# Kernel tuning notes

Measured on AMD Instinct MI355X. Metric: run time of the kernel, lower is better.

Reference implementation:

```python
import jax, jax.numpy as jnp
import numpy as np

SC = 19          # window stride/size (non-kitti)
K = 3 * SC       # 57, unfold kernel size
CH = 128         # chnn

def conv2d(x, w, b=None, pad=(0, 0)):
    y = jax.lax.conv_general_dilated(
        x, w, (1, 1), [(pad[0], pad[0]), (pad[1], pad[1])],
        dimension_numbers=('NCHW', 'OIHW', 'NCHW'))
    return y if b is None else y + b[None, :, None, None]

def unfold(x):
    # nn.Unfold(kernel_size=3*SC, padding=SC, stride=SC) -> [b, c, K*K, h_sc*w_sc]
    b, c, h, w = x.shape
    h_sc, w_sc = h // SC, w // SC
    xp = jnp.pad(x, ((0, 0), (0, 0), (SC, SC), (SC, SC)))
    ii = np.arange(h_sc)[:, None] * SC + np.arange(K)[None, :]
    jj = np.arange(w_sc)[:, None] * SC + np.arange(K)[None, :]
    p = xp[:, :, ii, :][:, :, :, :, jj]              # [b,c,h_sc,K,w_sc,K]
    return p.transpose(0, 1, 3, 5, 2, 4).reshape(b, c, K * K, h_sc * w_sc)

def to_windows(x):
    # [b,c,h,w] -> [b,c,h_sc*w_sc, SC*SC] (non-overlapping SCxSC windows)
    b, c, h, w = x.shape
    h_sc, w_sc = h // SC, w // SC
    return x.reshape(b, c, h_sc, SC, w_sc, SC).transpose(0, 1, 2, 4, 3, 5).reshape(b, c, h_sc * w_sc, SC * SC)

def fs_kernel(w_prelu, b, h, w):
    # geometric falloff kernel, separable in x/y: [b, K*K, L, SC*SC]
    a = w_prelu[0] * 0.02      # scp = 0.02
    half = 2.0 * SC            # half_ker
    crd = jnp.arange(K, dtype=jnp.float32)
    idx_x = SC + jnp.arange(w, dtype=jnp.float32) % SC
    idx_y = SC + jnp.arange(h, dtype=jnp.float32) % SC
    def falloff(d):
        v = d - half
        pre = jnp.where(v > 0, v, a * v)   # PReLU
        return jnp.maximum(1.0 - pre, 0.0) # -prelu + b(=1), clamped at 0
    ox = falloff(jnp.abs(crd[:, None] - idx_x[None, :]))  # [K, w]
    oy = falloff(jnp.abs(crd[:, None] - idx_y[None, :]))  # [K, h]
    ker = oy[:, None, :, None] * ox[None, :, None, :]      # [Ky, Kx, h, w]
    ker = jnp.broadcast_to(ker[None], (b, K, K, h, w)).reshape(b, K * K, h, w)
    return to_windows(ker)

def kpa(feat_ci, feat_mi, w_qk, w_v, gamma, w_prelu):
    b, c, h_in, w_in = feat_mi.shape
    x_pad = SC - w_in % SC
    y_pad = SC - h_in % SC
    pad4 = ((0, 0), (0, 0), (0, y_pad), (0, x_pad))
    feat_c = jnp.pad(feat_ci, pad4)
    feat_m = jnp.pad(feat_mi, pad4)
    h, w = h_in + y_pad, w_in + x_pad
    h_sc, w_sc = h // SC, w // SC
    # validity mask -> additive -99 bias for padded keys/queries
    fm = jnp.pad(jnp.ones((1, 1, h_in, w_in), feat_mi.dtype), pad4)
    fm_k = unfold(fm)                                  # [1,1,K^2,L]
    fm_q = to_windows(fm)                              # [1,1,L,SC^2]
    am = (fm_k[:, 0, :, :, None] * fm_q[:, 0, None, :, :] - 1.0) * 99.0
    # itr == 0 path: compute attention
    qk = conv2d(feat_c, w_qk)
    feat_q, feat_k = qk[:, :c], qk[:, c:]
    feat_k = unfold(feat_k) * (c ** -0.5)              # [b,c,K^2,L]
    feat_q = to_windows(feat_q)                        # [b,c,L,SC^2]
    attn = jnp.einsum('bckn,bcns->bkns', feat_k, feat_q) + am
    attn = jax.nn.softmax(fs_kernel(w_prelu, b, h, w) * attn, axis=1)
    feat_v = unfold(conv2d(feat_m, w_v))               # [b,c,K^2,L]
    feat_r = jnp.einsum('bkns,bckn->bcns', attn, feat_v)  # [b,c,L,SC^2]
    feat_r = feat_r.reshape(b, c, h_sc, w_sc, SC, SC).transpose(0, 1, 2, 4, 3, 5).reshape(b, c, h, w)
    return feat_mi + feat_r[:, :, :h_in, :w_in] * gamma[0]

def sep_conv_gru(h, x, wz1, bz1, wr1, br1, wq1, bq1, wz2, bz2, wr2, br2, wq2, bq2):
    hx = jnp.concatenate([h, x], 1)
    z = jax.nn.sigmoid(conv2d(hx, wz1, bz1, (0, 2)))
    r = jax.nn.sigmoid(conv2d(hx, wr1, br1, (0, 2)))
    q = jnp.tanh(conv2d(jnp.concatenate([r * h, x], 1), wq1, bq1, (0, 2)))
    h = (1 - z) * h + z * q
    hx = jnp.concatenate([h, x], 1)
    z = jax.nn.sigmoid(conv2d(hx, wz2, bz2, (2, 0)))
    r = jax.nn.sigmoid(conv2d(hx, wr2, br2, (2, 0)))
    q = jnp.tanh(conv2d(jnp.concatenate([r * h, x], 1), wq2, bq2, (2, 0)))
    return (1 - z) * h + z * q

PARAM_SHAPES = [
    ('w_cor1', (256, 324, 1, 1)), ('b_cor1', (256,)), ('w_cor2', (192, 256, 3, 3)), ('b_cor2', (192,)),
    ('w_flo1', (128, 2, 7, 7)), ('b_flo1', (128,)), ('w_flo2', (64, 128, 3, 3)), ('b_flo2', (64,)),
    ('w_mo', (126, 256, 3, 3)), ('b_mo', (126,)),
    ('w_qk', (256, 128, 1, 1)), ('w_v', (128, 128, 1, 1)),
    ('wz1', (128, 512, 1, 5)), ('bz1', (128,)), ('wr1', (128, 512, 1, 5)), ('br1', (128,)),
    ('wq1', (128, 512, 1, 5)), ('bq1', (128,)),
    ('wz2', (128, 512, 5, 1)), ('bz2', (128,)), ('wr2', (128, 512, 5, 1)), ('br2', (128,)),
    ('wq2', (128, 512, 5, 1)), ('bq2', (128,)),
    ('w_f1', (256, 128, 3, 3)), ('b_f1', (256,)), ('w_f2', (2, 256, 3, 3)), ('b_f2', (2,)),
    ('w_m1', (256, 128, 3, 3)), ('b_m1', (256,)), ('w_m2', (576, 256, 1, 1)), ('b_m2', (576,)),
]

def setup_inputs() -> dict:
    key = jax.random.key(0)
    B, H, W = 2, 55, 128
    ks = jax.random.split(key, len(PARAM_SHAPES) + 4)
    inp = {
        'net': jax.random.normal(ks[0], (B, CH, H, W), jnp.float32),
        'inp': jax.random.normal(ks[1], (B, CH, H, W), jnp.float32),
        'corr': jax.random.normal(ks[2], (B, 324, H, W), jnp.float32),
        'flow': jax.random.normal(ks[3], (B, 2, H, W), jnp.float32),
    }
    for i, (name, shp) in enumerate(PARAM_SHAPES):
        fan_in = int(np.prod(shp[1:])) if len(shp) > 1 else shp[0]
        scale = 1.0 / np.sqrt(fan_in) if len(shp) > 1 else 0.01
        inp[name] = scale * jax.random.normal(ks[4 + i], shp, jnp.float32)
    inp['gamma'] = jnp.array([0.5], jnp.float32)            # nonzero so KPA contributes
    inp['w_prelu'] = jnp.array([1.0 / 28.0], jnp.float32)    # 1 / h_k, h_k = (3*SC-1)/2
    inp['itr'] = 0
    return inp

def reference(net, inp, corr, flow, w_cor1, b_cor1, w_cor2, b_cor2, w_flo1, b_flo1, w_flo2, b_flo2, w_mo, b_mo, w_qk, w_v, wz1, bz1, wr1, br1, wq1, bq1, wz2, bz2, wr2, br2, wq2, bq2, w_f1, b_f1, w_f2, b_f2, w_m1, b_m1, w_m2, b_m2, gamma, w_prelu, itr):
    # _mo_enc
    fc = jax.nn.relu(conv2d(corr, w_cor1, b_cor1))
    fc = jax.nn.relu(conv2d(fc, w_cor2, b_cor2, (1, 1)))
    ff = jax.nn.relu(conv2d(flow, w_flo1, b_flo1, (3, 3)))
    ff = jax.nn.relu(conv2d(ff, w_flo2, b_flo2, (1, 1)))
    fm = jax.nn.relu(conv2d(jnp.concatenate([fc, ff], 1), w_mo, b_mo, (1, 1)))
    feat_mo = jnp.concatenate([fm, flow], 1)           # [b,128,h,w]
    # KPA attention (itr == 0)
    feat_moa = kpa(inp, feat_mo, w_qk, w_v, gamma, w_prelu)
    x = jnp.concatenate([inp, feat_mo, feat_moa], 1)   # [b,384,h,w]
    net = sep_conv_gru(net, x, wz1, bz1, wr1, br1, wq1, bq1, wz2, bz2, wr2, br2, wq2, bq2)
    d = jax.nn.relu(conv2d(net, w_f1, b_f1, (1, 1)))
    delta_flow = conv2d(d, w_f2, b_f2, (1, 1))
    m = jax.nn.relu(conv2d(net, w_m1, b_m1, (1, 1)))
    mask = 0.25 * conv2d(m, w_m2, b_m2)
    return net, mask, delta_flow
```

## Files before the change

kernel.cpp:

```cpp
#include <hip/hip_runtime.h>
#include <hip/hip_bf16.h>

typedef __bf16 bf16;
typedef __attribute__((ext_vector_type(8))) __bf16 v8bf;
typedef __attribute__((ext_vector_type(4))) float f32x4;
typedef __attribute__((ext_vector_type(16))) float f32x16;

#define HH 55
#define WW 128
#define HWP 7040
#define BHW 14080
#define QS 0.08838834764831845f
#define LOG2E 1.4426950408889634f

__device__ __forceinline__ void g2l16(const bf16* g, bf16* l){
  __builtin_amdgcn_global_load_lds(
      (const __attribute__((address_space(1))) void*)g,
      (__attribute__((address_space(3))) void*)l, 16, 0, 0);
}

#define NCV 19
__device__ const int PK_srcCS[NCV]  = {324,256,128,256,128,128,512,512,512,512,512,512,128,128,256,256,98,512,512};
__device__ const int PK_csv[NCV]    = {324,256,128,256,128,128,512,512,128,512,512,128,128,128,256,256,98,384,384};
__device__ const int PK_srcOff[NCV] = {0,0,0,0,0,0,0,0,0,0,0,0,0,0,0,0,0,128,128};
__device__ const int PK_wsrc[NCV]   = {0,1,2,3,4,5,6,7,8,9,10,11,12,13,14,15,16,8,11};
__device__ const int PK_Kc[NCV]     = {384,256,128,256,128,128,512,512,128,512,512,128,128,128,256,256,128,384,384};
__device__ const int PK_ntap[NCV]   = {1,9,9,9,1,1,5,5,5,5,5,5,9,9,9,1,1,5,5};
__device__ const int PK_Ctot[NCV]   = {256,256,128,128,256,128,256,256,128,256,256,128,512,512,128,640,128,128,128};
__device__ const int PK_coB[NCV]    = {0,0,0,0,0,0,0,128,0,0,128,0,0,256,0,0,0,0,0};
__device__ const int PK_dst[NCV]    = {0,98304,688128,835584,1130496,1163264,1179648,1179648,
  1835008,2162688,2162688,2818048,3145728,3145728,3735552,4030464,4194304,1916928,2899968};
__device__ const int PKD_cum[NCV+1] = {0,98304,540672,614400,904704,937472,953856,
  1281536,1609216,1691136,2018816,2346496,2428416,2723328,3018240,3022848,3170304,
  3186688,3432448,3678208};
__device__ const int PKD_Co[NCV]    = {256,192,64,126,256,128,128,128,128,128,128,128,256,256,2,576,128,128,128};

__device__ const int PB_off[15]={0,256,512,640,1152,1280,1408,1536,1664,1792,1920,2176,2432,2560,3200};
__device__ const int PB_cnt[15]={256,192,64,126,128,128,128,128,128,128,256,256,2,576,128};

struct W17 { const float* w[17]; };
struct B15 { const float* b[15]; };

struct XP {
  W17 wp; B15 bp;
  const float *net, *inp, *corr, *flow;
  bf16 *Bp; float *bias;
  bf16 *hx; float *hcur; bf16 *corr_cl; bf16 *im2c;
};

__global__ __launch_bounds__(256) void init_k(XP X){
  __shared__ float T[64][65];
  int bid = blockIdx.x;
  const int t = threadIdx.x;
  if (bid < 14368){
    int idx = bid*256 + t;
    int c = 0;
    while (idx >= PKD_cum[c+1]) ++c;
    int local = idx - PKD_cum[c];
    if (c == 16){
      int co = local >> 7, k = local & 127;
      if (k < 98)
        X.Bp[PK_dst[16] + co*128 + k] = (bf16)X.wp.w[16][co*98 + (k&1)*49 + (k>>1)];
      return;
    }
    int Kc = PK_Kc[c];
    int CKc = PKD_Co[c]*Kc;
    int tap = local / CKc;
    int rem = local - tap*CKc;
    int co = rem / Kc;
    int ci = rem - co*Kc;
    if (ci < PK_csv[c]){
      float v = X.wp.w[PK_wsrc[c]][(co*PK_srcCS[c] + PK_srcOff[c] + ci)*PK_ntap[c] + tap];
      if (c == 4 && co < 128) v *= QS;
      X.Bp[PK_dst[c] + (tap*PK_Ctot[c] + PK_coB[c] + co)*Kc + ci] = (bf16)v;
    }
    return;
  }
  bid -= 14368;
  if (bid < 880){
    int pt = bid%110, ct = (bid/110)&3, b = bid/440;
    const float* src = (ct < 2) ? X.net : X.inp;
    int c0s = (ct & 1)*64;
    int cbase = (ct < 2) ? 0 : 128;
    int p0 = pt*64;
    int pj = t & 63, cr4 = t >> 6;
#pragma unroll
    for (int i=0;i<16;++i)
      T[cr4 + i*4][pj] = src[((size_t)b*128 + c0s + cr4 + i*4)*HWP + p0 + pj];
    __syncthreads();
    int cj = t & 63, pr4 = t >> 6;
#pragma unroll
    for (int i=0;i<16;++i){
      int pp = p0 + pr4 + i*4;
      float v = T[cj][pr4 + i*4];
      X.hx[((size_t)(b*HWP+pp))*512 + cbase + c0s + cj] = (bf16)v;
      if (ct < 2) X.hcur[((size_t)(b*HWP+pp))*128 + c0s + cj] = v;
    }
    return;
  }
  bid -= 880;
  if (bid < 1320){
    int pt = bid%110, ct = (bid/110)%6, b = bid/660;
    int p0 = pt*64, c0s = ct*64;
    int pj = t & 63, cr4 = t >> 6;
#pragma unroll
    for (int i=0;i<16;++i){
      int c = c0s + cr4 + i*4;
      float v = 0.f;
      if (c < 324) v = X.corr[((size_t)b*324 + c)*HWP + p0 + pj];
      T[cr4 + i*4][pj] = v;
    }
    __syncthreads();
    int cj = t & 63, pr4 = t >> 6;
#pragma unroll
    for (int i=0;i<16;++i){
      int pp = p0 + pr4 + i*4;
      int cc = c0s + cj;
      X.corr_cl[((size_t)(b*HWP+pp))*384 + cc] = (bf16)T[cj][pr4 + i*4];
    }
    return;
  }
  bid -= 1320;
  if (bid < 110){
    int i = bid*256 + t;
    int c = i & 1, p = i >> 1;
    int b = p / HWP, pix = p - b*HWP;
    X.hx[(size_t)p*512 + 382 + c] = (bf16)X.flow[(b*2+c)*HWP + pix];
    return;
  }
  bid -= 110;
  if (bid < 7040){
    int i = bid*256 + t;
    int k = i & 127, p = i >> 7;
    int b = p / HWP, pix = p - b*HWP, y = pix >> 7, x = pix & 127;
    float v = 0.f;
    if (k < 98){
      int tap = k >> 1, c2 = k & 1, kh = tap/7, kw = tap - 7*(tap/7);
      int yy = y + kh - 3, xx = x + kw - 3;
      if ((unsigned)yy < 55u && (unsigned)xx < 128u) v = X.flow[(b*2+c2)*HWP + yy*128 + xx];
    }
    X.im2c[i] = (bf16)v;
    return;
  }
  for (int e=0;e<15;++e)
    for (int o=t; o<PB_cnt[e]; o+=256)
      X.bias[PB_off[e]+o] = X.bp.b[e][o];
}

__global__ __launch_bounds__(256) void transp_v(
    const bf16* __restrict__ src, bf16* __restrict__ dst)
{
  int pt = blockIdx.x, ct = blockIdx.y, b = blockIdx.z;
  __shared__ unsigned short T[64][66];
  int t = threadIdx.x;
  int p0 = pt*64, c0s = ct*64;
  int cj = t & 63, pr4 = t >> 6;
#pragma unroll
  for (int i=0;i<16;++i){
    int pp = p0 + pr4 + i*4;
    T[cj][pr4 + i*4] = ((const unsigned short*)src)[((size_t)(b*HWP+pp))*128 + c0s + cj];
  }
  __syncthreads();
  int pj = t & 63, cr4 = t >> 6;
#pragma unroll
  for (int i=0;i<16;++i){
    int cc = c0s + cr4 + i*4;
    ((unsigned short*)dst)[((size_t)(b*128 + cc))*HWP + p0 + pj] = T[cr4 + i*4][pj];
  }
}

struct GP {
  const bf16* A; const bf16* A2;
  const bf16* Bp; const float* bias;
  void* outp; const float* auxZ; float* auxH; float* auxN; const float* auxQ;
  int Astride, A2stride, Asplit;
  int outCtot, outC0, Nvalid, Kc, CtotPad, tapcode, act, outmode, ntiles, ntOff;
  float scale;
};

__global__ __launch_bounds__(256) void gemm_conv(GP ga, GP gb, GP gc, const bf16* __restrict__ zp)
{
  const int Mt = blockIdx.x;
  int nt = blockIdx.y;
  GP g;
  if (nt < ga.ntiles){ g = ga; }
  else if (nt < ga.ntiles + gb.ntiles){ g = gb; nt -= ga.ntiles; }
  else { g = gc; nt -= ga.ntiles + gb.ntiles; }
  const bf16* A        = g.A;
  const bf16* A2       = g.A2;
  const bf16* Bp       = g.Bp;
  const float* bias    = g.bias;
  void* outp           = g.outp;
  const float* auxZ    = g.auxZ;
  float* auxH          = g.auxH;
  float* auxN          = g.auxN;
  const float* auxQ    = g.auxQ;
  const int Astride    = g.Astride;
  const int A2stride   = g.A2stride;
  const int Asplit     = g.Asplit;
  const int outCtot    = g.outCtot;
  const int outC0      = g.outC0;
  const int Nvalid     = g.Nvalid;
  const int Kc         = g.Kc;
  const int CtotPad    = g.CtotPad;
  const int tapcode    = g.tapcode;
  const int act        = g.act;
  const int outmode    = g.outmode;
  const int ntOff      = g.ntOff;
  const float scale    = g.scale;

  const int bimg = Mt/110;
  const int rem = Mt - bimg*110;
  const int yy0 = rem >> 1;
  const int xh  = (rem & 1) << 6;
  const int tid = threadIdx.x;
  const int lane = tid & 63, wave = tid >> 6;
  const int wm = wave >> 1, wn = wave & 1;
  const int lr = lane & 15, lq2 = lane >> 4;

  __shared__ __align__(16) bf16 Al[2][4096];
  __shared__ __align__(16) bf16 Bl[2][8192];

  f32x4 acc[2][4];
#pragma unroll
  for (int m=0;m<2;++m)
#pragma unroll
    for (int n=0;n<4;++n) acc[m][n] = (f32x4){0.f,0.f,0.f,0.f};

  const int ntap = (tapcode==0) ? 1 : (tapcode==1 ? 9 : 5);
  const int nsteps = ntap*(Kc>>6);

  const int srow = tid >> 3;
  const int sc   = tid & 7;

#define STAGE(BUF, T, KC) { \
    int ddy, ddx; \
    if (tapcode==0){ ddy=0; ddx=0; } \
    else if (tapcode==1){ ddy=(T)/3-1; ddx=(T)-3*((T)/3)-1; } \
    else if (tapcode==2){ ddy=0; ddx=(T)-2; } \
    else { ddy=(T)-2; ddx=0; } \
    int ysrc = yy0 + ddy; \
    bool yok = (unsigned)ysrc < 55u; \
    const bf16* Abase; int Astr; \
    if ((KC) < Asplit){ Astr = A2stride; \
      Abase = A2 + (size_t)((bimg*55+ysrc)*128)*Astr + (KC); } \
    else { Astr = Astride; \
      Abase = A + (size_t)((bimg*55+ysrc)*128)*Astr + (KC); } \
    _Pragma("unroll") \
    for (int is=0; is<2; ++is){ \
      int r = is*32 + srow; \
      int cc = sc ^ (r&7); \
      int gx = xh + r + ddx; \
      const bf16* srcp = (yok && (unsigned)gx < 128u) ? \
          (Abase + (size_t)gx*Astr + cc*8) : (zp + cc*8); \
      g2l16(srcp, &Al[BUF][is*2048 + wave*512]); \
    } \
    const bf16* Bt = Bp + (size_t)((T)*CtotPad + (nt+ntOff)*128)*Kc + (KC); \
    _Pragma("unroll") \
    for (int is=0; is<4; ++is){ \
      int r = is*32 + srow; \
      int cc = sc ^ (r&7); \
      g2l16(Bt + (size_t)r*Kc + cc*8, &Bl[BUF][is*2048 + wave*512]); \
    } }

  STAGE(0, 0, 0);
  __syncthreads();

  int tcur = 0, kcc = 0;
  for (int si=0; si<nsteps; ++si){
    int kn = kcc + 64, tn = tcur;
    if (kn == Kc){ kn = 0; tn = tcur + 1; }
    if (si + 1 < nsteps){ STAGE((si+1)&1, tn, kn); }
    __builtin_amdgcn_sched_barrier(0);
    kcc = kn; tcur = tn;
    const bf16* Ac = Al[si&1];
    const bf16* Bc = Bl[si&1];
#pragma unroll
    for (int kk=0; kk<2; ++kk){
      v8bf af[2], bfr[4];
#pragma unroll
      for (int m=0;m<2;++m){
        int row = wm*32 + m*16 + lr;
        af[m] = *(const v8bf*)(Ac + row*64 + (((kk*4+lq2) ^ (row&7))<<3));
      }
#pragma unroll
      for (int n=0;n<4;++n){
        int row = wn*64 + n*16 + lr;
        bfr[n] = *(const v8bf*)(Bc + row*64 + (((kk*4+lq2) ^ (row&7))<<3));
      }
#pragma unroll
      for (int m=0;m<2;++m)
#pragma unroll
        for (int n=0;n<4;++n)
          acc[m][n] = __builtin_amdgcn_mfma_f32_16x16x32_bf16(af[m], bfr[n], acc[m][n], 0,0,0);
    }
    __syncthreads();
  }
#undef STAGE

  const size_t pixbase = (size_t)(bimg*55 + yy0)*128 + xh;
  if (outmode == 0){
    bf16* Ost = (bf16*)Al;
#pragma unroll
    for (int nn=0; nn<4; ++nn){
      int colL = wn*64 + nn*16 + lr;
      float bvl = bias[(nt+ntOff)*128 + colL];
#pragma unroll
      for (int m=0;m<2;++m){
        int rowx = wm*32 + m*16 + lq2*4;
        f32x4 v = acc[m][nn];
#pragma unroll
        for (int r=0;r<4;++r){
          float vv = v[r] + bvl;
          if (act==1)      vv = fmaxf(vv, 0.f);
          else if (act==2) vv = 1.f/(1.f+__expf(-vv));
          else if (act==3) vv = tanhf(vv);
          vv *= scale;
          int row = rowx + r;
          int pch = (colL>>3) ^ (row & 7);
          Ost[row*128 + (pch<<3) + (colL&7)] = (bf16)vv;
        }
      }
    }
    __syncthreads();
    {
      int rowl = tid >> 2, seg = tid & 3;
      size_t p = pixbase + rowl;
      bf16* dstp = (bf16*)outp + p*outCtot + outC0 + (nt+ntOff)*128 + seg*32;
      const bf16* srcr = Ost + rowl*128;
      int cb = (nt+ntOff)*128 + seg*32;
#pragma unroll
      for (int k2=0;k2<4;++k2){
        int pch = (seg*4 + k2) ^ (rowl & 7);
        int cog = cb + k2*8;
        if (cog + 8 <= Nvalid)
          *(uint4*)(dstp + k2*8) = *(const uint4*)(srcr + (pch<<3));
        else if (cog < Nvalid){
          const bf16* s8 = srcr + (pch<<3);
          for (int e=0; e<Nvalid-cog; ++e) dstp[k2*8+e] = s8[e];
        }
      }
    }
  } else if (outmode == 2){
    float* Ost2 = (float*)Bl;
#pragma unroll
    for (int nn=0; nn<4; ++nn){
      int chL = wn*64 + nn*16 + lr;
      float bvl = bias[(nt+ntOff)*128 + chL];
#pragma unroll
      for (int m=0;m<2;++m){
        int rowx = wm*32 + m*16 + lq2*4;
        f32x4 v = acc[m][nn];
#pragma unroll
        for (int r=0;r<4;++r){
          float vv = v[r] + bvl;
          if (act==1)      vv = fmaxf(vv, 0.f);
          else if (act==2) vv = 1.f/(1.f+__expf(-vv));
          else if (act==3) vv = tanhf(vv);
          Ost2[chL*64 + rowx + r] = vv*scale;
        }
      }
    }
    __syncthreads();
    {
      int ch = tid >> 1, half = tid & 1;
      int cog = (nt+ntOff)*128 + ch;
      if (cog < Nvalid){
        float* dstp = (float*)outp + ((size_t)bimg*outCtot + outC0 + cog)*HWP
                    + yy0*128 + xh + half*32;
        const float* srcr = Ost2 + ch*64 + half*32;
#pragma unroll
        for (int k2=0;k2<8;++k2)
          *(uint4*)(dstp + k2*4) = *(const uint4*)(srcr + k2*4);
      }
    }
  } else {
#pragma unroll
    for (int nn=0; nn<4; ++nn){
      int cog = (nt+ntOff)*128 + wn*64 + nn*16 + lr;
      float bvl = bias[cog];
      bool cok = cog < Nvalid;
#pragma unroll
      for (int m=0;m<2;++m){
        int rowx = wm*32 + m*16 + lq2*4;
        f32x4 v = acc[m][nn];
#pragma unroll
        for (int r=0;r<4;++r){
          int prow = rowx + r;
          size_t p = pixbase + prow;
          float vv = v[r] + bvl;
          if (outmode==4 && auxQ) vv += auxQ[p*128 + cog];
          if (act==1)      vv = fmaxf(vv, 0.f);
          else if (act==2) vv = 1.f/(1.f+__expf(-vv));
          else if (act==3) vv = tanhf(vv);
          vv *= scale;
          if (cok){
            if (outmode==1) ((float*)outp)[p*outCtot + outC0 + cog] = vv;
            else if (outmode==3){
              int c = cog & 127;
              ((bf16*)outp)[p*128 + c] = (bf16)(vv * auxH[p*128 + c]);
            } else {
              int c = cog;
              float z  = auxZ[p*128 + c];
              float h0 = auxH[p*128 + c];
              float hn = (1.f - z)*h0 + z*vv;
              auxH[p*128 + c] = hn;
              ((bf16*)outp)[p*512 + c] = (bf16)hn;
              if (auxN){
                int pixloc = (int)(p - (size_t)bimg*HWP);
                auxN[((size_t)bimg*128 + c)*HWP + pixloc] = hn;
              }
            }
          }
        }
      }
    }
  }
}

__global__ __launch_bounds__(256,1) void attn_k(
    const bf16* __restrict__ QK, const bf16* __restrict__ Vt,
    bf16* __restrict__ hx,
    const float* __restrict__ gammap, const float* __restrict__ wprelup)
{
  __shared__ __align__(16) float SM[16640];
  const int tid = threadIdx.x;
  const int wv = tid >> 6, lane = tid & 63;
  const int lq = lane & 31, hi = lane >> 5;
  const int blk = blockIdx.x;
  const int qt = blk % 12;
  const int n  = (blk/12) % 21;
  const int b  = blk / 252;
  const int hs = n/7, wd = n - 7*hs;
  const int y0 = (hs-1)*19, x0 = (wd-1)*19;
  const int rylo = max(0, y0), ryhi = min(54, y0+56);
  const int rxlo = max(0, x0), rxhi = min(127, x0+56);
  const int rxA  = rxlo & ~7;
  const int s = qt*32 + lq;
  const int sy = s/19, sx = s - sy*19;
  const int qy = y0 + 19 + sy, qx = x0 + 19 + sx;
  const int qpix = (b*55 + min(qy,54))*128 + min(qx,127);
  const float a = wprelup[0]*0.02f;
  const float qyf = (float)qy;

  bf16* Kl = (bf16*)SM + wv*8192;
  bf16* Vl = Kl + 4096;

  v8bf qf[8];
#pragma unroll
  for (int ks=0; ks<8; ++ks)
    qf[ks] = *(const v8bf*)(QK + (size_t)qpix*256 + ks*16 + hi*8);

  float fx0[16], fx1[16];
  unsigned msk0 = 0, msk1 = 0;
  {
    float dxq0 = (float)(rxA - qx);
    int xl0 = rxlo - rxA, xm0 = rxhi - rxA;
#pragma unroll
    for (int r=0;r<16;++r){
      int Ri = (r&3) + 8*(r>>2) + 4*hi;
      float dxv = fabsf(dxq0 + (float)Ri) - 38.f;
      fx0[r] = fmaxf(1.f - fmaxf(dxv, a*dxv), 0.f);
      if (Ri >= xl0 && Ri <= xm0) msk0 |= 1u<<r;
      float dxv1 = fabsf(dxq0 + 32.f + (float)Ri) - 38.f;
      fx1[r] = fmaxf(1.f - fmaxf(dxv1, a*dxv1), 0.f);
      int Ri1 = Ri + 32;
      if (Ri1 >= xl0 && Ri1 <= xm0) msk1 |= 1u<<r;
    }
  }

  f32x16 acc[4];
#pragma unroll
  for (int nf=0; nf<4; ++nf)
#pragma unroll
    for (int r=0;r<16;++r) acc[nf][r] = 0.f;
  float m2 = -40.f, den = 0.f;

  const int nry = (ryhi - rylo - wv)/4 + 1;
  const int nit = nry*2;

#define ISSUE_K(RY, RX) { int pixK = (b*55+(RY))*128 + (RX); \
  _Pragma("unroll") \
  for (int i=0;i<8;++i){ \
    int key = i*4 + (lane>>4); int cs = (lane&15) ^ (key&7); \
    g2l16(QK + (size_t)(pixK+key)*256 + 128 + cs*8, Kl + i*512); } }
#define ISSUE_V(RY, RX) { \
  _Pragma("unroll") \
  for (int i=0;i<8;++i){ \
    int ch = i*16 + (lane>>2); int cs = (lane&3) ^ ((ch>>1)&3); \
    g2l16(Vt + (size_t)(b*128+ch)*HWP + (RY)*128 + (RX) + cs*8, Vl + i*512); } }

  ISSUE_K(rylo + wv, rxA);

  for (int it=0; it<nit; ++it){
    const int ry  = rylo + wv + (it>>1)*4;
    const int tpar = it & 1;
    asm volatile("s_waitcnt lgkmcnt(0)" ::: "memory");
    __builtin_amdgcn_sched_barrier(0);
    asm volatile("s_waitcnt vmcnt(0)" ::: "memory");
    __builtin_amdgcn_sched_barrier(0);
    ISSUE_V(ry, rxA + tpar*32);
    __builtin_amdgcn_sched_barrier(0);

    f32x16 Cs;
#pragma unroll
    for (int r=0;r<16;++r) Cs[r] = 0.f;
#pragma unroll
    for (int ks=0; ks<8; ++ks){
      v8bf kf = *(const v8bf*)(Kl + lq*128 + (((ks*2+hi) ^ (lq&7))<<3));
      Cs = __builtin_amdgcn_mfma_f32_32x32x16_bf16(kf, qf[ks], Cs, 0,0,0);
    }
    float pr[16];
    {
      float dyv = fabsf((float)ry - qyf) - 38.f;
      float fy = fmaxf(1.f - fmaxf(dyv, a*dyv), 0.f);
      float fyk = fy * LOG2E;
      unsigned mk = tpar ? msk1 : msk0;
      float l2v[16]; float tmax = -1e30f;
#pragma unroll
      for (int r=0;r<16;++r){
        float fx = tpar ? fx1[r] : fx0[r];
        float lv = fyk * fx * Cs[r];
        lv = ((mk>>r)&1u) ? lv : -1e30f;
        l2v[r] = lv;
        tmax = fmaxf(tmax, lv);
      }
      tmax = fmaxf(tmax, __shfl_xor(tmax, 32));
      if (__any(tmax > m2 + 11.f)){
        float m2n = fmaxf(m2, tmax);
        float sc = exp2f(m2 - m2n);
        den *= sc;
#pragma unroll
        for (int r=0;r<16;++r){
          float scr = __shfl(sc, (r&3) + 8*(r>>2) + 4*hi);
          acc[0][r]*=scr; acc[1][r]*=scr; acc[2][r]*=scr; acc[3][r]*=scr;
        }
        m2 = m2n;
      }
#pragma unroll
      for (int r=0;r<16;++r){
        pr[r] = exp2f(l2v[r] - m2);
        den += pr[r];
      }
    }
    asm volatile("s_waitcnt lgkmcnt(0)" ::: "memory");
    __builtin_amdgcn_sched_barrier(0);
    asm volatile("s_waitcnt vmcnt(0)" ::: "memory");
    __builtin_amdgcn_sched_barrier(0);
    if (it + 1 < nit){
      int ryn = rylo + wv + ((it+1)>>1)*4;
      ISSUE_K(ryn, rxA + ((it+1)&1)*32);
      __builtin_amdgcn_sched_barrier(0);
    }
    float po[8], po2[8];
#pragma unroll
    for (int r=0;r<8;++r) po[r]  = __shfl_xor(pr[r],   32);
#pragma unroll
    for (int r=0;r<8;++r) po2[r] = __shfl_xor(pr[r+8], 32);
    v8bf pa0, pa1;
#pragma unroll
    for (int j=0;j<4;++j){
      pa0[j]   = (bf16)(hi ? po[j+4]  : pr[j]);
      pa0[j+4] = (bf16)(hi ? pr[j+4]  : po[j]);
      pa1[j]   = (bf16)(hi ? po2[j+4] : pr[j+8]);
      pa1[j+4] = (bf16)(hi ? pr[j+12] : po2[j]);
    }
#pragma unroll
    for (int nf=0; nf<4; ++nf){
      int ch = nf*32 + lq;
      int sw = (lq>>1)&3;
      v8bf v0 = *(const v8bf*)(Vl + ch*32 + ((hi     ^ sw)<<3));
      v8bf v1 = *(const v8bf*)(Vl + ch*32 + (((2+hi) ^ sw)<<3));
      acc[nf] = __builtin_amdgcn_mfma_f32_32x32x16_bf16(pa0, v0, acc[nf], 0,0,0);
      acc[nf] = __builtin_amdgcn_mfma_f32_32x32x16_bf16(pa1, v1, acc[nf], 0,0,0);
    }
  }
#undef ISSUE_K
#undef ISSUE_V
  den += __shfl_xor(den, 32);

  float* Osh = SM;
  float* Msh = SM + 16384;
  float* Dsh = SM + 16512;
  __syncthreads();
#pragma unroll
  for (int nf=0; nf<4; ++nf)
#pragma unroll
    for (int r=0;r<16;++r)
      Osh[(wv*32 + (r&3) + 8*(r>>2) + 4*hi)*128 + nf*32 + lq] = acc[nf][r];
  if (hi == 0){ Msh[wv*32 + lq] = m2; Dsh[wv*32 + lq] = den; }
  __syncthreads();

  int q = tid >> 3, co = (tid & 7)*16;
  float m0 = Msh[q], m1 = Msh[32+q], mm2 = Msh[64+q], m3 = Msh[96+q];
  float M = fmaxf(fmaxf(m0,m1), fmaxf(mm2,m3));
  float s0 = exp2f(m0-M), s1 = exp2f(m1-M), s2 = exp2f(mm2-M), s3 = exp2f(m3-M);
  int ss = qt*32 + q;
  float dent = s0*Dsh[q] + s1*Dsh[32+q] + s2*Dsh[64+q] + s3*Dsh[96+q];
  int sy2 = ss/19, sx2 = ss - sy2*19;
  int qy2 = y0 + 19 + sy2, qx2 = x0 + 19 + sx2;
  if (ss < 361 && qy2 < 55 && qx2 < 128){
    size_t pix = (size_t)(b*55+qy2)*128 + qx2;
    float g = gammap[0] / dent;
#pragma unroll
    for (int c=0;c<16;++c){
      float o = s0*Osh[q*128+co+c] + s1*Osh[(32+q)*128+co+c]
              + s2*Osh[(64+q)*128+co+c] + s3*Osh[(96+q)*128+co+c];
      float fm = (float)hx[pix*512 + 256 + co + c];
      hx[pix*512 + 384 + co + c] = (bf16)(fm + o*g);
    }
  }
}

static inline GP mkgp(const bf16* A, int Astride, const bf16* Bp, const float* bias,
                      void* outp, int outCtot, int outC0, int Nvalid, int Kc, int CtotPad,
                      int tapcode, int act, int outmode, float scale, int ntiles){
  GP g{};
  g.A=A; g.A2=A; g.Astride=Astride; g.A2stride=Astride; g.Asplit=0;
  g.Bp=Bp; g.bias=bias; g.outp=outp;
  g.auxZ=nullptr; g.auxH=nullptr; g.auxN=nullptr; g.auxQ=nullptr;
  g.outCtot=outCtot; g.outC0=outC0; g.Nvalid=Nvalid; g.Kc=Kc; g.CtotPad=CtotPad;
  g.tapcode=tapcode; g.act=act; g.outmode=outmode; g.ntiles=ntiles; g.ntOff=0;
  g.scale=scale;
  return g;
}

extern "C" void kernel_launch(void* const* d_in, const int* in_sizes, int n_in,
                              void* d_out, int out_size, void* d_ws, size_t ws_size,
                              hipStream_t stream) {
  const float* net   = (const float*)d_in[0];
  const float* inp   = (const float*)d_in[1];
  const float* corr  = (const float*)d_in[2];
  const float* flow  = (const float*)d_in[3];
  const float* w_cor1=(const float*)d_in[4];  const float* b_cor1=(const float*)d_in[5];
  const float* w_cor2=(const float*)d_in[6];  const float* b_cor2=(const float*)d_in[7];
  const float* w_flo1=(const float*)d_in[8];  const float* b_flo1=(const float*)d_in[9];
  const float* w_flo2=(const float*)d_in[10]; const float* b_flo2=(const float*)d_in[11];
  const float* w_mo  =(const float*)d_in[12]; const float* b_mo  =(const float*)d_in[13];
  const float* w_qk  =(const float*)d_in[14];
  const float* w_v   =(const float*)d_in[15];
  const float* wz1=(const float*)d_in[16]; const float* bz1=(const float*)d_in[17];
  const float* wr1=(const float*)d_in[18]; const float* br1=(const float*)d_in[19];
  const float* wq1=(const float*)d_in[20]; const float* bq1=(const float*)d_in[21];
  const float* wz2=(const float*)d_in[22]; const float* bz2=(const float*)d_in[23];
  const float* wr2=(const float*)d_in[24]; const float* br2=(const float*)d_in[25];
  const float* wq2=(const float*)d_in[26]; const float* bq2=(const float*)d_in[27];
  const float* w_f1=(const float*)d_in[28]; const float* b_f1=(const float*)d_in[29];
  const float* w_f2=(const float*)d_in[30]; const float* b_f2=(const float*)d_in[31];
  const float* w_m1=(const float*)d_in[32]; const float* b_m1=(const float*)d_in[33];
  const float* w_m2=(const float*)d_in[34]; const float* b_m2=(const float*)d_in[35];
  const float* gamma  =(const float*)d_in[36];
  const float* w_prelu=(const float*)d_in[37];

  float* ws = (float*)d_ws;
  bf16* hx     = (bf16*)ws;
  bf16* BPp    = (bf16*)(ws + 3604480);
  float* BIASp = ws + 5709824;
  const bf16* zp = (const bf16*)(ws + 5713152);
  float* ZB0   = ws + 5713216;
  const size_t S0 = 5713344;
  bf16* corr_cl = (bf16*)(ws + S0);
  bf16* fc1o    = (bf16*)(ws + S0 + 2703360);
  bf16* catB    = (bf16*)(ws + S0 + 4505600);
  bf16* ff1o    = (bf16*)(ws + S0 + 6307840);
  bf16* im2c    = (bf16*)(ws + S0 + 7208960);
  float* hcur   = ws + S0 + 8110080;
  bf16* QKb    = (bf16*)(ws + S0);
  bf16* Vb     = (bf16*)(ws + S0 + 1810432);
  bf16* Vt     = (bf16*)(ws + S0 + 2711552);
  float* zb    = ws + S0;
  float* qpart = ws + S0 + 1802240;
  bf16* rhb    = (bf16*)(ws + S0 + 3604480);
  bf16* dm     = (bf16*)(ws + S0);

  float* out_net  = (float*)d_out;
  float* out_mask = out_net + 1802240;
  float* out_df   = out_net + 9912320;

  dim3 blk(256);

  hipMemsetAsync(ws + 3604480, 0, (size_t)8435456, stream);
  XP X{};
  const float* wl[17] = {w_cor1,w_cor2,w_flo2,w_mo,w_qk,w_v,wz1,wr1,wq1,wz2,wr2,wq2,w_f1,w_m1,w_f2,w_m2,w_flo1};
  const float* bl[15] = {b_cor1,b_cor2,b_flo2,b_mo,bz1,br1,bq1,bz2,br2,bq2,b_f1,b_m1,b_f2,b_m2,b_flo1};
  for (int i=0;i<17;++i) X.wp.w[i]=wl[i];
  for (int i=0;i<15;++i) X.bp.b[i]=bl[i];
  X.net=net; X.inp=inp; X.corr=corr; X.flow=flow;
  X.Bp=BPp; X.bias=BIASp; X.hx=hx; X.hcur=hcur; X.corr_cl=corr_cl; X.im2c=im2c;
  init_k<<<dim3(14368+880+1320+110+7040+1),blk,0,stream>>>(X);

  GP g0{};

  {
    GP a = mkgp(corr_cl,384, BPp+0,       BIASp+0,    fc1o,256,0,256, 384,256, 0,1,0,1.f, 2);
    GP b = mkgp(im2c,128,    BPp+4194304, BIASp+3200, ff1o,128,0,128, 128,128, 0,1,0,1.f, 1);
    gemm_conv<<<dim3(220,3),blk,0,stream>>>(a, b, g0, zp);
  }
  {
    GP a = mkgp(fc1o,256,    BPp+98304,   BIASp+256,  catB,256,0,192, 256,256, 1,1,0,1.f, 2);
    GP b = mkgp(ff1o,128,    BPp+688128,  BIASp+512,  catB,256,192,64,128,128, 1,1,0,1.f, 1);
    gemm_conv<<<dim3(220,3),blk,0,stream>>>(a, b, g0, zp);
  }
  {
    GP a = mkgp(catB,256,    BPp+835584,  BIASp+640,  hx,  512,256,126,256,128, 1,1,0,1.f, 1);
    gemm_conv<<<dim3(220,1),blk,0,stream>>>(a, g0, g0, zp);
  }

  {
    GP a = mkgp(hx+128,512,  BPp+1130496, BIASp+768,  QKb, 256,0,256, 128,256, 0,0,0,1.f, 2);
    GP b = mkgp(hx+256,512,  BPp+1163264, BIASp+1024, Vb,  128,0,128, 128,128, 0,0,0,1.f, 1);
    gemm_conv<<<dim3(220,3),blk,0,stream>>>(a, b, g0, zp);
  }
  transp_v<<<dim3(110,2,2),blk,0,stream>>>(Vb, Vt);
  attn_k<<<dim3(504),blk,0,stream>>>(QKb, Vt, hx, gamma, w_prelu);

  {
    GP a = mkgp(hx,512,      BPp+1179648, BIASp+1152, zb,  128,0,128, 512,256, 2,2,1,1.f, 1);
    GP b = mkgp(hx,512,      BPp+1179648, BIASp+1152, rhb, 0,0,256,   512,256, 2,2,3,1.f, 1);
    b.ntOff = 1; b.auxH = hcur;
    GP c = mkgp(hx+128,512,  BPp+1916928, ZB0,        qpart,128,0,128,384,128, 2,0,1,1.f, 1);
    gemm_conv<<<dim3(220,3),blk,0,stream>>>(a, b, c, zp);
  }
  {
    GP a = mkgp(rhb,128,     BPp+1835008, BIASp+1408, hx,  0,0,128,   128,128, 2,3,4,1.f, 1);
    a.auxZ = zb; a.auxH = hcur; a.auxN = nullptr; a.auxQ = qpart;
    gemm_conv<<<dim3(220,1),blk,0,stream>>>(a, g0, g0, zp);
  }

  {
    GP a = mkgp(hx,512,      BPp+2162688, BIASp+1536, zb,  128,0,128, 512,256, 3,2,1,1.f, 1);
    GP b = mkgp(hx,512,      BPp+2162688, BIASp+1536, rhb, 0,0,256,   512,256, 3,2,3,1.f, 1);
    b.ntOff = 1; b.auxH = hcur;
    GP c = mkgp(hx+128,512,  BPp+2899968, ZB0,        qpart,128,0,128,384,128, 3,0,1,1.f, 1);
    gemm_conv<<<dim3(220,3),blk,0,stream>>>(a, b, c, zp);
  }
  {
    GP a = mkgp(rhb,128,     BPp+2818048, BIASp+1792, hx,  0,0,128,   128,128, 3,3,4,1.f, 1);
    a.auxZ = zb; a.auxH = hcur; a.auxN = out_net; a.auxQ = qpart;
    gemm_conv<<<dim3(220,1),blk,0,stream>>>(a, g0, g0, zp);
  }

  {
    GP a = mkgp(hx,512,      BPp+3145728, BIASp+1920, dm,  512,0,512, 128,512, 1,1,0,1.f, 4);
    gemm_conv<<<dim3(220,4),blk,0,stream>>>(a, g0, g0, zp);
  }
  {
    GP a = mkgp(dm+256,512,  BPp+4030464, BIASp+2560, out_mask,576,0,576,256,640, 0,0,2,0.25f, 5);
    GP b = mkgp(dm,512,      BPp+3735552, BIASp+2432, out_df,  2,  0,2,  256,128, 1,0,2,1.f,   1);
    gemm_conv<<<dim3(220,6),blk,0,stream>>>(a, b, g0, zp);
  }
}
```

Before: 521.7 us.

## Fuse V transpose into GEMM epilogue, merge QK launch, use permlane swap

Adds a GEMM epilogue mode that writes the V projection straight into channel-major bf16 layout through shared memory, which removes the separate transpose kernel and its intermediate buffer. The QK projection GEMM is merged into the same launch as the motion-encoder output conv, and V gets its own launch after it. In the attention kernel, the shuffle-based repacking of probabilities to bf16 is replaced with packed bf16 conversion and v_permlane32_swap. The reordering assumes the QK GEMM reads hx+128 channels that are not written by the merged conv in the same launch, which looks valid because that conv writes to offset 256.

Result: faster. 500.1 us (-4.1%).

```diff
diff --git a/kernel.cpp b/kernel.cpp
--- a/kernel.cpp
+++ b/kernel.cpp
@@ -145,28 +145,6 @@
   for (int e=0;e<15;++e)
     for (int o=t; o<PB_cnt[e]; o+=256)
       X.bias[PB_off[e]+o] = X.bp.b[e][o];
-}
-
-__global__ __launch_bounds__(256) void transp_v(
-    const bf16* __restrict__ src, bf16* __restrict__ dst)
-{
-  int pt = blockIdx.x, ct = blockIdx.y, b = blockIdx.z;
-  __shared__ unsigned short T[64][66];
-  int t = threadIdx.x;
-  int p0 = pt*64, c0s = ct*64;
-  int cj = t & 63, pr4 = t >> 6;
-#pragma unroll
-  for (int i=0;i<16;++i){
-    int pp = p0 + pr4 + i*4;
-    T[cj][pr4 + i*4] = ((const unsigned short*)src)[((size_t)(b*HWP+pp))*128 + c0s + cj];
-  }
-  __syncthreads();
-  int pj = t & 63, cr4 = t >> 6;
-#pragma unroll
-  for (int i=0;i<16;++i){
-    int cc = c0s + cr4 + i*4;
-    ((unsigned short*)dst)[((size_t)(b*128 + cc))*HWP + p0 + pj] = T[cr4 + i*4][pj];
-  }
 }
 
 struct GP {
@@ -374,6 +352,31 @@
           *(uint4*)(dstp + k2*4) = *(const uint4*)(srcr + k2*4);
       }
     }
+  } else if (outmode == 5){
+    bf16* Ost3 = (bf16*)Bl;
+#pragma unroll
+    for (int nn=0; nn<4; ++nn){
+      int chL = wn*64 + nn*16 + lr;
+      float bvl = bias[(nt+ntOff)*128 + chL];
+#pragma unroll
+      for (int m=0;m<2;++m){
+        int rowx = wm*32 + m*16 + lq2*4;
+        f32x4 v = acc[m][nn];
+#pragma unroll
+        for (int r=0;r<4;++r)
+          Ost3[chL*72 + rowx + r] = (bf16)(v[r] + bvl);
+      }
+    }
+    __syncthreads();
+    {
+      int ch = tid >> 1, half = tid & 1;
+      bf16* dstp = (bf16*)outp + ((size_t)bimg*outCtot + outC0 + ch)*HWP
+                 + yy0*128 + xh + half*32;
+      const bf16* srcr = Ost3 + ch*72 + half*32;
+#pragma unroll
+      for (int k2=0;k2<4;++k2)
+        *(uint4*)(dstp + k2*8) = *(const uint4*)(srcr + k2*8);
+    }
   } else {
 #pragma unroll
     for (int nn=0; nn<4; ++nn){
@@ -552,19 +555,23 @@
       ISSUE_K(ryn, rxA + ((it+1)&1)*32);
       __builtin_amdgcn_sched_barrier(0);
     }
-    float po[8], po2[8];
-#pragma unroll
-    for (int r=0;r<8;++r) po[r]  = __shfl_xor(pr[r],   32);
-#pragma unroll
-    for (int r=0;r<8;++r) po2[r] = __shfl_xor(pr[r+8], 32);
-    v8bf pa0, pa1;
-#pragma unroll
-    for (int j=0;j<4;++j){
-      pa0[j]   = (bf16)(hi ? po[j+4]  : pr[j]);
-      pa0[j+4] = (bf16)(hi ? pr[j+4]  : po[j]);
-      pa1[j]   = (bf16)(hi ? po2[j+4] : pr[j+8]);
-      pa1[j+4] = (bf16)(hi ? pr[j+12] : po2[j]);
-    }
+    unsigned w0,w1,w2,w3,w4,w5,w6,w7;
+    asm("v_cvt_pk_bf16_f32 %0, %1, %2" : "=v"(w0) : "v"(pr[0]),  "v"(pr[1]));
+    asm("v_cvt_pk_bf16_f32 %0, %1, %2" : "=v"(w1) : "v"(pr[2]),  "v"(pr[3]));
+    asm("v_cvt_pk_bf16_f32 %0, %1, %2" : "=v"(w2) : "v"(pr[4]),  "v"(pr[5]));
+    asm("v_cvt_pk_bf16_f32 %0, %1, %2" : "=v"(w3) : "v"(pr[6]),  "v"(pr[7]));
+    asm("v_cvt_pk_bf16_f32 %0, %1, %2" : "=v"(w4) : "v"(pr[8]),  "v"(pr[9]));
+    asm("v_cvt_pk_bf16_f32 %0, %1, %2" : "=v"(w5) : "v"(pr[10]), "v"(pr[11]));
+    asm("v_cvt_pk_bf16_f32 %0, %1, %2" : "=v"(w6) : "v"(pr[12]), "v"(pr[13]));
+    asm("v_cvt_pk_bf16_f32 %0, %1, %2" : "=v"(w7) : "v"(pr[14]), "v"(pr[15]));
+    asm("v_permlane32_swap_b32 %0, %1" : "+v"(w0), "+v"(w2));
+    asm("v_permlane32_swap_b32 %0, %1" : "+v"(w1), "+v"(w3));
+    asm("v_permlane32_swap_b32 %0, %1" : "+v"(w4), "+v"(w6));
+    asm("v_permlane32_swap_b32 %0, %1" : "+v"(w5), "+v"(w7));
+    union { unsigned u[4]; v8bf v; } U0, U1;
+    U0.u[0]=w0; U0.u[1]=w1; U0.u[2]=w2; U0.u[3]=w3;
+    U1.u[0]=w4; U1.u[1]=w5; U1.u[2]=w6; U1.u[3]=w7;
+    v8bf pa0 = U0.v, pa1 = U1.v;
 #pragma unroll
     for (int nf=0; nf<4; ++nf){
       int ch = nf*32 + lq;
@@ -666,7 +673,6 @@
   bf16* im2c    = (bf16*)(ws + S0 + 7208960);
   float* hcur   = ws + S0 + 8110080;
   bf16* QKb    = (bf16*)(ws + S0);
-  bf16* Vb     = (bf16*)(ws + S0 + 1810432);
   bf16* Vt     = (bf16*)(ws + S0 + 2711552);
   float* zb    = ws + S0;
   float* qpart = ws + S0 + 1802240;
@@ -701,17 +707,16 @@
     GP b = mkgp(ff1o,128,    BPp+688128,  BIASp+512,  catB,256,192,64,128,128, 1,1,0,1.f, 1);
     gemm_conv<<<dim3(220,3),blk,0,stream>>>(a, b, g0, zp);
   }
+
   {
     GP a = mkgp(catB,256,    BPp+835584,  BIASp+640,  hx,  512,256,126,256,128, 1,1,0,1.f, 1);
+    GP b = mkgp(hx+128,512,  BPp+1130496, BIASp+768,  QKb, 256,0,256, 128,256, 0,0,0,1.f, 2);
+    gemm_conv<<<dim3(220,3),blk,0,stream>>>(a, b, g0, zp);
+  }
+  {
+    GP a = mkgp(hx+256,512,  BPp+1163264, BIASp+1024, Vt,  128,0,128, 128,128, 0,0,5,1.f, 1);
     gemm_conv<<<dim3(220,1),blk,0,stream>>>(a, g0, g0, zp);
   }
-
-  {
-    GP a = mkgp(hx+128,512,  BPp+1130496, BIASp+768,  QKb, 256,0,256, 128,256, 0,0,0,1.f, 2);
-    GP b = mkgp(hx+256,512,  BPp+1163264, BIASp+1024, Vb,  128,0,128, 128,128, 0,0,0,1.f, 1);
-    gemm_conv<<<dim3(220,3),blk,0,stream>>>(a, b, g0, zp);
-  }
-  transp_v<<<dim3(110,2,2),blk,0,stream>>>(Vb, Vt);
   attn_k<<<dim3(504),blk,0,stream>>>(QKb, Vt, hx, gamma, w_prelu);
 
   {
```
